# Kernel optimization log

Hardware: AMD Instinct MI355X
Metric: run time of the kernel (lower is better)

The kernel has to match this reference:

```python
import jax, jax.numpy as jnp
import numpy as np

N_NODES = 100000
N_EDGES = 1600000
IN_CH = 64
OUT_CH = 64
NUM_K = 9  # (degree+1)^dim = 3*3 quadratic B-spline taps; equals prod(kernel_size) here


def _quad_basis(v):
    # torch_spline_conv quadratic basis for k_mod in {0,1,2}; v = frac(pseudo*(K-deg)) = pseudo here
    return jnp.stack([0.5 * v * v - v + 0.5,
                      -v * v + v + 0.5,
                      0.5 * v * v], axis=-1)  # [E,3]


def spline_conv(x, src, dst, pseudo, W, root, bias, n_nodes):
    # W: [9, C_in, C_out]; basis B: [E, 9]
    b0 = _quad_basis(pseudo[:, 0])          # [E,3]
    b1 = _quad_basis(pseudo[:, 1])          # [E,3]
    B = (b0[:, :, None] * b1[:, None, :]).reshape(pseudo.shape[0], NUM_K)  # [E,9]
    x_src = x[src]                           # gather [E, C_in]
    msg = B[:, 0:1] * (x_src @ W[0])
    for k in range(1, NUM_K):                # fixed small loop over kernel taps
        msg = msg + B[:, k:k + 1] * (x_src @ W[k])
    out = jax.ops.segment_sum(msg, dst, num_segments=n_nodes)  # scatter-add at targets
    return out + x @ root + bias


def setup_inputs() -> dict:
    key = jax.random.key(0)
    ks = jax.random.split(key, 10)
    x = jax.random.normal(ks[0], (N_NODES, IN_CH), dtype=jnp.float32)
    edge_index = jax.random.randint(ks[1], (2, N_EDGES), 0, N_NODES, dtype=jnp.int64)
    pseudo = jax.random.uniform(ks[2], (N_EDGES, 2), dtype=jnp.float32)
    s1 = 1.0 / np.sqrt(IN_CH * NUM_K)
    s2 = 1.0 / np.sqrt(OUT_CH * NUM_K)
    W1 = jax.random.normal(ks[3], (NUM_K, IN_CH, OUT_CH), dtype=jnp.float32) * s1
    root1 = jax.random.normal(ks[4], (IN_CH, OUT_CH), dtype=jnp.float32) * s1
    b1 = jax.random.normal(ks[5], (OUT_CH,), dtype=jnp.float32) * 0.01
    W2 = jax.random.normal(ks[6], (NUM_K, OUT_CH, OUT_CH), dtype=jnp.float32) * s2
    root2 = jax.random.normal(ks[7], (OUT_CH, OUT_CH), dtype=jnp.float32) * s2
    b2 = jax.random.normal(ks[8], (OUT_CH,), dtype=jnp.float32) * 0.01
    return {"x": x, "edge_index": edge_index, "pseudo": pseudo,
            "W1": W1, "root1": root1, "b1": b1,
            "W2": W2, "root2": root2, "b2": b2}


def reference(x, edge_index, pseudo, W1, root1, b1, W2, root2, b2):
    src, dst = edge_index[0], edge_index[1]  # PyG: aggregate messages at target
    h = jax.nn.relu(spline_conv(x, src, dst, pseudo, W1, root1, b1, N_NODES))
    h = jax.nn.relu(spline_conv(h, src, dst, pseudo, W2, root2, b2, N_NODES))
    return h
```

## Files before the change

### kernel.cpp

```cpp
#include <hip/hip_runtime.h>
#include <stdint.h>

typedef __attribute__((ext_vector_type(8))) short bf16x8;
typedef __attribute__((ext_vector_type(4))) float f32x4;

__device__ __forceinline__ float bf2f(unsigned short u) {
  union { unsigned int i; float f; } x; x.i = ((unsigned int)u) << 16; return x.f;
}
__device__ __forceinline__ unsigned short f2bf(float f) {
  union { float f; unsigned int i; } x; x.f = f;
  unsigned int i = x.i;
  return (unsigned short)((i + 0x7FFFu + ((i >> 16) & 1u)) >> 16);
}
__device__ __forceinline__ float f16lo(unsigned int u) {
  union { unsigned short s; _Float16 h; } x; x.s = (unsigned short)(u & 0xFFFFu);
  return (float)x.h;
}
__device__ __forceinline__ float f16hi(unsigned int u) {
  union { unsigned short s; _Float16 h; } x; x.s = (unsigned short)(u >> 16);
  return (float)x.h;
}
__device__ __forceinline__ unsigned int packf16(float a, float b) {
  union { unsigned short s; _Float16 h; } x, y;
  x.h = (_Float16)a; y.h = (_Float16)b;
  return (unsigned int)x.s | ((unsigned int)y.s << 16);
}


__global__ void count_kernel(const int* __restrict__ ei, int E, int* __restrict__ counts) {
  int e = blockIdx.x * blockDim.x + threadIdx.x;
  if (e < E) atomicAdd(&counts[ei[E + e]], 1);
}

__global__ void scan1_kernel(const int* __restrict__ counts, int n, int* __restrict__ bsum) {
  int i = blockIdx.x * 256 + threadIdx.x;
  int v = (i < n) ? counts[i] : 0;
  int lane = threadIdx.x & 63, w = threadIdx.x >> 6;
  for (int d = 32; d > 0; d >>= 1) v += __shfl_down(v, d, 64);
  __shared__ int ws[4];
  if (lane == 0) ws[w] = v;
  __syncthreads();
  if (threadIdx.x == 0) bsum[blockIdx.x] = ws[0] + ws[1] + ws[2] + ws[3];
}

__global__ void scan2_kernel(int* __restrict__ bsum, int G) {
  int t = threadIdx.x;
  int c = (G + 511) >> 9;
  int lo = min(t * c, G), hi = min(lo + c, G);
  int s = 0;
  for (int i = lo; i < hi; ++i) s += bsum[i];
  int lane = t & 63, w = t >> 6;
  int incl = s;
  for (int d = 1; d < 64; d <<= 1) { int u = __shfl_up(incl, d, 64); if (lane >= d) incl += u; }
  __shared__ int wsum[8];
  if (lane == 63) wsum[w] = incl;
  __syncthreads();
  int wpre = 0;
  for (int i = 0; i < w; ++i) wpre += wsum[i];
  int excl = wpre + incl - s;
  for (int i = lo; i < hi; ++i) { int v = bsum[i]; bsum[i] = excl; excl += v; }
}

__global__ void scan3_kernel(const int* __restrict__ counts, int n, const int* __restrict__ bsum,
                             int* __restrict__ offsets, int* __restrict__ cursor, int total) {
  int i = blockIdx.x * 256 + threadIdx.x;
  int v = (i < n) ? counts[i] : 0;
  int lane = threadIdx.x & 63, w = threadIdx.x >> 6;
  int incl = v;
  for (int d = 1; d < 64; d <<= 1) { int u = __shfl_up(incl, d, 64); if (lane >= d) incl += u; }
  __shared__ int wsum[4];
  if (lane == 63) wsum[w] = incl;
  __syncthreads();
  int pre = bsum[blockIdx.x];
  for (int j = 0; j < w; ++j) pre += wsum[j];
  if (i < n) {
    int excl = pre + incl - v;
    offsets[i] = excl;
    cursor[i] = excl;
  }
  if (i == 0) offsets[n] = total;
}


__global__ void fill_kernel(const int* __restrict__ ei, const float* __restrict__ pseudo,
                            int E, int* __restrict__ cursor, uint4* __restrict__ recs) {
  int e = blockIdx.x * blockDim.x + threadIdx.x;
  if (e >= E) return;
  int d = ei[E + e];
  int s = ei[e];
  float2 uv = ((const float2*)pseudo)[e];
  float u = uv.x, v = uv.y;
  float b0 = 0.5f * u * u - u + 0.5f, b1 = -u * u + u + 0.5f, b2 = 0.5f * u * u;
  float c0 = 0.5f * v * v - v + 0.5f, c1 = -v * v + v + 0.5f, c2 = 0.5f * v * v;
  int p = atomicAdd(&cursor[d], 1);
  uint4 r;
  r.x = ((unsigned int)s) << 7;
  r.y = packf16(b0, b1);
  r.z = packf16(b2, c0);
  r.w = packf16(c1, c2);
  recs[p] = r;
}


__global__ void wconv_kernel(const float* __restrict__ W, const float* __restrict__ root,
                             unsigned short* __restrict__ Wt) {
  int i = blockIdx.x * blockDim.x + threadIdx.x;
  if (i >= 640 * 64) return;
  int co = i / 640, r = i % 640;
  float v = (r < 576) ? W[r * 64 + co] : root[(r - 576) * 64 + co];
  Wt[i] = f2bf(v);
}


__global__ void xconv_kernel(const float4* __restrict__ x4, ushort4* __restrict__ xh4, int n4) {
  int i = blockIdx.x * blockDim.x + threadIdx.x;
  if (i < n4) {
    float4 v = x4[i];
    ushort4 o;
    o.x = f2bf(v.x); o.y = f2bf(v.y); o.z = f2bf(v.z); o.w = f2bf(v.w);
    xh4[i] = o;
  }
}


#define SROW 648
#define CAP 288

#define UNPACK_FMA(RY, RZ, RW, XV)                                 \
  {                                                                \
    float b0 = f16lo(RY), b1 = f16hi(RY), b2 = f16lo(RZ);          \
    float c0 = f16hi(RZ), c1 = f16lo(RW), c2 = f16hi(RW);          \
    float t0 = b0 * (XV), t1 = b1 * (XV), t2 = b2 * (XV);          \
    a0 += t0 * c0; a1 += t0 * c1; a2 += t0 * c2;                   \
    a3 += t1 * c0; a4 += t1 * c1; a5 += t1 * c2;                   \
    a6 += t2 * c0; a7 += t2 * c1; a8 += t2 * c2;                   \
  }

template <bool OUTBF16>
__global__ __launch_bounds__(512) void fused_kernel(const int* __restrict__ offsets,
                                                    const uint4* __restrict__ recs,
                                                    const unsigned short* __restrict__ Xh,
                                                    const unsigned short* __restrict__ Wt,
                                                    const float* __restrict__ bias,
                                                    void* __restrict__ outv, int N) {
  __shared__ __align__(16) short sA[16 * SROW];
  __shared__ __align__(16) uint4 sRec[CAP];
  __shared__ __align__(16) unsigned short sXg[CAP * 64];
  int tid = threadIdx.x, w = tid >> 6, lane = tid & 63;
  int nodeBase = blockIdx.x * 16;
  int nTop = min(nodeBase + 16, N);
  const char* Xb = (const char*)Xh;
  unsigned int laneB = (unsigned int)lane * 2u;

  int blockBeg = offsets[nodeBase];
  int blockEnd = offsets[nTop];
  int stage = min(blockEnd - blockBeg, CAP);

  for (int i = tid; i < stage; i += 512) sRec[i] = recs[(size_t)blockBeg + i];
  __syncthreads();
  {
    int chunk = tid & 7;
    int rbase = tid >> 3;
    for (int r0 = 0; r0 < stage; r0 += 64) {
      int r = r0 + rbase;
      if (r < stage) {
        unsigned int so = sRec[r].x;
        uint4 v = *(const uint4*)(Xb + so + chunk * 16);
        *(uint4*)((char*)sXg + r * 128 + chunk * 16) = v;
      }
    }
  }
  __syncthreads();

#pragma unroll
  for (int t = 0; t < 2; ++t) {
    int row = w * 2 + t;
    int n = nodeBase + row;
    if (n < N) {
      int beg = __builtin_amdgcn_readfirstlane(offsets[n]);
      int end = __builtin_amdgcn_readfirstlane(offsets[n + 1]);
      unsigned short selfu = Xh[(size_t)n * 64 + lane];
      float a0 = 0.f, a1 = 0.f, a2 = 0.f, a3 = 0.f, a4 = 0.f,
            a5 = 0.f, a6 = 0.f, a7 = 0.f, a8 = 0.f;
      int lbeg = beg - blockBeg;
      int lend = end - blockBeg;
      int lcap = min(lend, CAP);
      int m = lcap - lbeg;
      for (int j0 = 0; j0 < m; j0 += 4) {
#pragma unroll
        for (int k = 0; k < 4; ++k) {
          int idx = j0 + k;
          int le = lbeg + (idx < m ? idx : 0);
          uint4 r = sRec[le];
          float xv = bf2f(sXg[le * 64 + lane]);
          if (idx >= m) { r.y = 0u; r.z = 0u; r.w = 0u; }
          UNPACK_FMA(r.y, r.z, r.w, xv)
        }
      }
      for (int j = (lbeg > lcap ? lbeg : lcap); j < lend; ++j) {
        uint4 r = recs[(size_t)blockBeg + j];
        float xv = bf2f(*(const unsigned short*)(Xb + r.x + laneB));
        UNPACK_FMA(r.y, r.z, r.w, xv)
      }
      int rb = row * SROW;
      sA[rb + 0 * 64 + lane] = (short)f2bf(a0);
      sA[rb + 1 * 64 + lane] = (short)f2bf(a1);
      sA[rb + 2 * 64 + lane] = (short)f2bf(a2);
      sA[rb + 3 * 64 + lane] = (short)f2bf(a3);
      sA[rb + 4 * 64 + lane] = (short)f2bf(a4);
      sA[rb + 5 * 64 + lane] = (short)f2bf(a5);
      sA[rb + 6 * 64 + lane] = (short)f2bf(a6);
      sA[rb + 7 * 64 + lane] = (short)f2bf(a7);
      sA[rb + 8 * 64 + lane] = (short)f2bf(a8);
      sA[rb + 576 + lane] = (short)selfu;
    }
  }
  __syncthreads();

  if (w < 4) {
    int r15 = lane & 15, kg = lane >> 4;
    f32x4 acc = {0.f, 0.f, 0.f, 0.f};
#pragma unroll
    for (int kk = 0; kk < 20; ++kk) {
      int kbase = kk * 32 + kg * 8;
      bf16x8 af = *(const bf16x8*)(&sA[r15 * SROW + kbase]);
      bf16x8 bfr = *(const bf16x8*)(Wt + (size_t)(w * 16 + r15) * 640 + kbase);
      acc = __builtin_amdgcn_mfma_f32_16x16x32_bf16(af, bfr, acc, 0, 0, 0);
    }
    int col = w * 16 + r15;
    float bv = bias[col];
    int row0 = kg * 4;
#pragma unroll
    for (int r = 0; r < 4; ++r) {
      int node = nodeBase + row0 + r;
      if (node < N) {
        float val = fmaxf(acc[r] + bv, 0.f);
        size_t idx = (size_t)node * 64 + col;
        if (OUTBF16) ((unsigned short*)outv)[idx] = f2bf(val);
        else ((float*)outv)[idx] = val;
      }
    }
  }
}


extern "C" void kernel_launch(void* const* d_in, const int* in_sizes, int n_in,
                              void* d_out, int out_size, void* d_ws, size_t ws_size,
                              hipStream_t stream) {
  const float* x = (const float*)d_in[0];
  const int* ei = (const int*)d_in[1];
  const float* pseudo = (const float*)d_in[2];
  const float* W1 = (const float*)d_in[3];
  const float* root1 = (const float*)d_in[4];
  const float* b1 = (const float*)d_in[5];
  const float* W2 = (const float*)d_in[6];
  const float* root2 = (const float*)d_in[7];
  const float* b2 = (const float*)d_in[8];

  const int N = in_sizes[0] / 64;
  const int E = in_sizes[1] / 2;
  const int G = (N + 255) / 256;

  char* p = (char*)d_ws;
  auto carve = [&](size_t bytes) -> void* {
    void* r = (void*)p;
    p += (bytes + 255) & ~(size_t)255;
    return r;
  };
  int* counts = (int*)carve((size_t)N * 4);
  int* offsets = (int*)carve((size_t)(N + 1) * 4);
  int* cursor = (int*)carve((size_t)N * 4);
  int* bsum = (int*)carve((size_t)G * 4);
  uint4* recs = (uint4*)carve((size_t)E * 16);
  unsigned short* Wt1 = (unsigned short*)carve(640 * 64 * 2);
  unsigned short* Wt2 = (unsigned short*)carve(640 * 64 * 2);
  unsigned short* h = (unsigned short*)carve((size_t)N * 64 * 2);
  unsigned short* xh = (unsigned short*)carve((size_t)N * 64 * 2);
  (void)ws_size;

  hipMemsetAsync(counts, 0, (size_t)N * 4, stream);
  count_kernel<<<(E + 255) / 256, 256, 0, stream>>>(ei, E, counts);
  scan1_kernel<<<G, 256, 0, stream>>>(counts, N, bsum);
  scan2_kernel<<<1, 512, 0, stream>>>(bsum, G);
  scan3_kernel<<<G, 256, 0, stream>>>(counts, N, bsum, offsets, cursor, E);
  fill_kernel<<<(E + 255) / 256, 256, 0, stream>>>(ei, pseudo, E, cursor, recs);
  wconv_kernel<<<160, 256, 0, stream>>>(W1, root1, Wt1);
  wconv_kernel<<<160, 256, 0, stream>>>(W2, root2, Wt2);
  xconv_kernel<<<(N * 16 + 255) / 256, 256, 0, stream>>>((const float4*)x, (ushort4*)xh, N * 16);

  int FB = (N + 15) / 16;
  fused_kernel<true><<<FB, 512, 0, stream>>>(offsets, recs, xh, Wt1, b1, (void*)h, N);
  fused_kernel<false><<<FB, 512, 0, stream>>>(offsets, recs, h, Wt2, b2, d_out, N);
}
```

Baseline: 520.8 us.

## Split block edges evenly across waves with LDS atomic flush per destination

Each block's edges are now divided evenly among the 8 waves instead of one wave per destination row. This targets load imbalance from skewed in-degrees. Each wave accumulates the 9 basis-weighted sums and flushes them to an fp32 LDS tile with atomic adds whenever the destination changes, using destination low bits packed into the record. The staged gathered-X buffer is removed in favour of direct global gathers with software double-buffering, CAP is raised, and the LDS tile is converted to bf16 before the MFMA. The trade is extra LDS atomics, more global-gather latency, and fp32 LDS storage.

```diff
diff --git a/kernel.cpp b/kernel.cpp
--- a/kernel.cpp
+++ b/kernel.cpp
@@ -24,6 +24,11 @@
   union { unsigned short s; _Float16 h; } x, y;
   x.h = (_Float16)a; y.h = (_Float16)b;
   return (unsigned int)x.s | ((unsigned int)y.s << 16);
+}
+__device__ __forceinline__ unsigned int cvtpk_bf16(float lo, float hi) {
+  unsigned int d;
+  asm("v_cvt_pk_bf16_f32 %0, %1, %2" : "=v"(d) : "v"(lo), "v"(hi));
+  return d;
 }
 
 
@@ -94,7 +99,7 @@
   float c0 = 0.5f * v * v - v + 0.5f, c1 = -v * v + v + 0.5f, c2 = 0.5f * v * v;
   int p = atomicAdd(&cursor[d], 1);
   uint4 r;
-  r.x = ((unsigned int)s) << 7;
+  r.x = (((unsigned int)s) << 7) | ((unsigned int)d & 127u);
   r.y = packf16(b0, b1);
   r.z = packf16(b2, c0);
   r.w = packf16(c1, c2);
@@ -123,8 +128,8 @@
 }
 
 
-#define SROW 648
-#define CAP 288
+#define SAFROW 644
+#define CAP 384
 
 #define UNPACK_FMA(RY, RZ, RW, XV)                                 \
   {                                                                \
@@ -136,16 +141,58 @@
     a6 += t2 * c0; a7 += t2 * c1; a8 += t2 * c2;                   \
   }
 
+#define FLUSH(C)                                                             \
+  {                                                                          \
+    float* fb_ = &sAf[(C) * SAFROW + lane];                                  \
+    atomicAdd(fb_ + 0,   a0); atomicAdd(fb_ + 64,  a1);                      \
+    atomicAdd(fb_ + 128, a2); atomicAdd(fb_ + 192, a3);                      \
+    atomicAdd(fb_ + 256, a4); atomicAdd(fb_ + 320, a5);                      \
+    atomicAdd(fb_ + 384, a6); atomicAdd(fb_ + 448, a7);                      \
+    atomicAdd(fb_ + 512, a8);                                                \
+    a0 = a1 = a2 = a3 = a4 = a5 = a6 = a7 = a8 = 0.f;                        \
+  }
+
+#define LOADG(J, R0, R1, R2, R3, X0, X1, X2, X3)                             \
+  {                                                                          \
+    R0 = sRec[(J)]; R1 = sRec[(J) + 1]; R2 = sRec[(J) + 2]; R3 = sRec[(J) + 3]; \
+    X0 = *(const unsigned short*)(Xb + (R0.x & 0xFFFFFF80u) + laneB);        \
+    X1 = *(const unsigned short*)(Xb + (R1.x & 0xFFFFFF80u) + laneB);        \
+    X2 = *(const unsigned short*)(Xb + (R2.x & 0xFFFFFF80u) + laneB);        \
+    X3 = *(const unsigned short*)(Xb + (R3.x & 0xFFFFFF80u) + laneB);        \
+  }
+
+#define PROCG(R0, R1, R2, R3, X0, X1, X2, X3)                                \
+  {                                                                          \
+    int d0_ = __builtin_amdgcn_readfirstlane(R0.x) & 15;                     \
+    int d1_ = __builtin_amdgcn_readfirstlane(R1.x) & 15;                     \
+    int d2_ = __builtin_amdgcn_readfirstlane(R2.x) & 15;                     \
+    int d3_ = __builtin_amdgcn_readfirstlane(R3.x) & 15;                     \
+    if (d0_ == cur && d1_ == cur && d2_ == cur && d3_ == cur) {              \
+      UNPACK_FMA(R0.y, R0.z, R0.w, bf2f(X0))                                 \
+      UNPACK_FMA(R1.y, R1.z, R1.w, bf2f(X1))                                 \
+      UNPACK_FMA(R2.y, R2.z, R2.w, bf2f(X2))                                 \
+      UNPACK_FMA(R3.y, R3.z, R3.w, bf2f(X3))                                 \
+    } else {                                                                 \
+      if (d0_ != cur) { FLUSH(cur) cur = d0_; }                              \
+      UNPACK_FMA(R0.y, R0.z, R0.w, bf2f(X0))                                 \
+      if (d1_ != cur) { FLUSH(cur) cur = d1_; }                              \
+      UNPACK_FMA(R1.y, R1.z, R1.w, bf2f(X1))                                 \
+      if (d2_ != cur) { FLUSH(cur) cur = d2_; }                              \
+      UNPACK_FMA(R2.y, R2.z, R2.w, bf2f(X2))                                 \
+      if (d3_ != cur) { FLUSH(cur) cur = d3_; }                              \
+      UNPACK_FMA(R3.y, R3.z, R3.w, bf2f(X3))                                 \
+    }                                                                        \
+  }
+
 template <bool OUTBF16>
-__global__ __launch_bounds__(512) void fused_kernel(const int* __restrict__ offsets,
-                                                    const uint4* __restrict__ recs,
-                                                    const unsigned short* __restrict__ Xh,
-                                                    const unsigned short* __restrict__ Wt,
-                                                    const float* __restrict__ bias,
-                                                    void* __restrict__ outv, int N) {
-  __shared__ __align__(16) short sA[16 * SROW];
+__global__ __launch_bounds__(512, 6) void fused_kernel(const int* __restrict__ offsets,
+                                                       const uint4* __restrict__ recs,
+                                                       const unsigned short* __restrict__ Xh,
+                                                       const unsigned short* __restrict__ Wt,
+                                                       const float* __restrict__ bias,
+                                                       void* __restrict__ outv, int N) {
+  __shared__ __align__(16) float sAf[16 * SAFROW];
   __shared__ __align__(16) uint4 sRec[CAP];
-  __shared__ __align__(16) unsigned short sXg[CAP * 64];
   int tid = threadIdx.x, w = tid >> 6, lane = tid & 63;
   int nodeBase = blockIdx.x * 16;
   int nTop = min(nodeBase + 16, N);
@@ -157,62 +204,72 @@
   int stage = min(blockEnd - blockBeg, CAP);
 
   for (int i = tid; i < stage; i += 512) sRec[i] = recs[(size_t)blockBeg + i];
-  __syncthreads();
-  {
-    int chunk = tid & 7;
-    int rbase = tid >> 3;
-    for (int r0 = 0; r0 < stage; r0 += 64) {
-      int r = r0 + rbase;
-      if (r < stage) {
-        unsigned int so = sRec[r].x;
-        uint4 v = *(const uint4*)(Xb + so + chunk * 16);
-        *(uint4*)((char*)sXg + r * 128 + chunk * 16) = v;
-      }
-    }
-  }
-  __syncthreads();
-
+  for (int i = tid; i < 16 * 144; i += 512) {
+    int r = i / 144, c = i - r * 144;
+    *(f32x4*)(&sAf[r * SAFROW + c * 4]) = (f32x4){0.f, 0.f, 0.f, 0.f};
+  }
 #pragma unroll
   for (int t = 0; t < 2; ++t) {
     int row = w * 2 + t;
     int n = nodeBase + row;
-    if (n < N) {
-      int beg = __builtin_amdgcn_readfirstlane(offsets[n]);
-      int end = __builtin_amdgcn_readfirstlane(offsets[n + 1]);
-      unsigned short selfu = Xh[(size_t)n * 64 + lane];
+    if (n < nTop) sAf[row * SAFROW + 576 + lane] = bf2f(Xh[(size_t)n * 64 + lane]);
+  }
+  __syncthreads();
+
+  {
+    int chunk = (stage + 7) >> 3;
+    int cBeg = w * chunk;
+    int cEnd = min(stage, cBeg + chunk);
+    if (cBeg < cEnd) {
       float a0 = 0.f, a1 = 0.f, a2 = 0.f, a3 = 0.f, a4 = 0.f,
             a5 = 0.f, a6 = 0.f, a7 = 0.f, a8 = 0.f;
-      int lbeg = beg - blockBeg;
-      int lend = end - blockBeg;
-      int lcap = min(lend, CAP);
-      int m = lcap - lbeg;
-      for (int j0 = 0; j0 < m; j0 += 4) {
+      int cur = __builtin_amdgcn_readfirstlane(sRec[cBeg].x) & 15;
+      int i = cBeg;
+      int nfull = (cEnd - cBeg) >> 2;
+      uint4 r0, r1, r2, r3, s0, s1, s2, s3;
+      unsigned short px0, px1, px2, px3, py0, py1, py2, py3;
+      if (nfull > 0) { LOADG(i, r0, r1, r2, r3, px0, px1, px2, px3) }
+      int g = 0;
+      while (g < nfull) {
+        if (g + 1 < nfull) { LOADG(i + 4, s0, s1, s2, s3, py0, py1, py2, py3) }
+        PROCG(r0, r1, r2, r3, px0, px1, px2, px3)
+        i += 4; ++g;
+        if (g >= nfull) break;
+        if (g + 1 < nfull) { LOADG(i + 4, r0, r1, r2, r3, px0, px1, px2, px3) }
+        PROCG(s0, s1, s2, s3, py0, py1, py2, py3)
+        i += 4; ++g;
+      }
+      for (; i < cEnd; ++i) {
+        uint4 rr = sRec[i];
+        unsigned short xv = *(const unsigned short*)(Xb + (rr.x & 0xFFFFFF80u) + laneB);
+        int dd = __builtin_amdgcn_readfirstlane(rr.x) & 15;
+        if (dd != cur) { FLUSH(cur) cur = dd; }
+        UNPACK_FMA(rr.y, rr.z, rr.w, bf2f(xv))
+      }
+      FLUSH(cur)
+    }
+    if (blockEnd - blockBeg > CAP) {
+      int gcap = blockBeg + CAP;
 #pragma unroll
-        for (int k = 0; k < 4; ++k) {
-          int idx = j0 + k;
-          int le = lbeg + (idx < m ? idx : 0);
-          uint4 r = sRec[le];
-          float xv = bf2f(sXg[le * 64 + lane]);
-          if (idx >= m) { r.y = 0u; r.z = 0u; r.w = 0u; }
-          UNPACK_FMA(r.y, r.z, r.w, xv)
+      for (int t = 0; t < 2; ++t) {
+        int row = w * 2 + t;
+        int n = nodeBase + row;
+        if (n < nTop) {
+          int beg = __builtin_amdgcn_readfirstlane(offsets[n]);
+          int end = __builtin_amdgcn_readfirstlane(offsets[n + 1]);
+          int s = beg > gcap ? beg : gcap;
+          if (s < end) {
+            float a0 = 0.f, a1 = 0.f, a2 = 0.f, a3 = 0.f, a4 = 0.f,
+                  a5 = 0.f, a6 = 0.f, a7 = 0.f, a8 = 0.f;
+            for (int j = s; j < end; ++j) {
+              uint4 rr = recs[j];
+              unsigned short xv = *(const unsigned short*)(Xb + (rr.x & 0xFFFFFF80u) + laneB);
+              UNPACK_FMA(rr.y, rr.z, rr.w, bf2f(xv))
+            }
+            FLUSH(row)
+          }
         }
       }
-      for (int j = (lbeg > lcap ? lbeg : lcap); j < lend; ++j) {
-        uint4 r = recs[(size_t)blockBeg + j];
-        float xv = bf2f(*(const unsigned short*)(Xb + r.x + laneB));
-        UNPACK_FMA(r.y, r.z, r.w, xv)
-      }
-      int rb = row * SROW;
-      sA[rb + 0 * 64 + lane] = (short)f2bf(a0);
-      sA[rb + 1 * 64 + lane] = (short)f2bf(a1);
-      sA[rb + 2 * 64 + lane] = (short)f2bf(a2);
-      sA[rb + 3 * 64 + lane] = (short)f2bf(a3);
-      sA[rb + 4 * 64 + lane] = (short)f2bf(a4);
-      sA[rb + 5 * 64 + lane] = (short)f2bf(a5);
-      sA[rb + 6 * 64 + lane] = (short)f2bf(a6);
-      sA[rb + 7 * 64 + lane] = (short)f2bf(a7);
-      sA[rb + 8 * 64 + lane] = (short)f2bf(a8);
-      sA[rb + 576 + lane] = (short)selfu;
     }
   }
   __syncthreads();
@@ -223,9 +280,15 @@
 #pragma unroll
     for (int kk = 0; kk < 20; ++kk) {
       int kbase = kk * 32 + kg * 8;
-      bf16x8 af = *(const bf16x8*)(&sA[r15 * SROW + kbase]);
+      f32x4 v0 = *(const f32x4*)(&sAf[r15 * SAFROW + kbase]);
+      f32x4 v1 = *(const f32x4*)(&sAf[r15 * SAFROW + kbase + 4]);
+      union { unsigned int u[4]; bf16x8 v8; } af;
+      af.u[0] = cvtpk_bf16(v0[0], v0[1]);
+      af.u[1] = cvtpk_bf16(v0[2], v0[3]);
+      af.u[2] = cvtpk_bf16(v1[0], v1[1]);
+      af.u[3] = cvtpk_bf16(v1[2], v1[3]);
       bf16x8 bfr = *(const bf16x8*)(Wt + (size_t)(w * 16 + r15) * 640 + kbase);
-      acc = __builtin_amdgcn_mfma_f32_16x16x32_bf16(af, bfr, acc, 0, 0, 0);
+      acc = __builtin_amdgcn_mfma_f32_16x16x32_bf16(af.v8, bfr, acc, 0, 0, 0);
     }
     int col = w * 16 + r15;
     float bv = bias[col];
```

Measured after the change: 1.188 ms. 128% more time.

## Stream edges per warp across four nodes with software-pipelined gathers

Applied to the files above, without the earlier changes.

Drops the LDS staging of edge records and gathered source rows. Each wave now walks the contiguous edge range of four consecutive nodes, with records and feature loads prefetched three edges ahead in a rotating pipeline. A packed low-bit destination tag in the record marks node boundaries, and the accumulators are flushed to shared memory whenever the node changes. Blocks shrink to 256 threads and LDS use drops, which allows more blocks per CU, but the scalar tag check and a zero-init pass add work in the inner loop.

```diff
diff --git a/kernel.cpp b/kernel.cpp
--- a/kernel.cpp
+++ b/kernel.cpp
@@ -94,7 +94,7 @@
   float c0 = 0.5f * v * v - v + 0.5f, c1 = -v * v + v + 0.5f, c2 = 0.5f * v * v;
   int p = atomicAdd(&cursor[d], 1);
   uint4 r;
-  r.x = ((unsigned int)s) << 7;
+  r.x = (((unsigned int)s) << 7) | ((unsigned int)d & 127u);
   r.y = packf16(b0, b1);
   r.z = packf16(b2, c0);
   r.w = packf16(c1, c2);
@@ -124,100 +124,111 @@
 
 
 #define SROW 648
-#define CAP 288
-
-#define UNPACK_FMA(RY, RZ, RW, XV)                                 \
+
+#define GX(R) (*(const unsigned short*)(Xb + ((R).x & 0xFFFFFF80u) + laneB))
+
+#define FLUSHROW(C)                                                \
   {                                                                \
-    float b0 = f16lo(RY), b1 = f16hi(RY), b2 = f16lo(RZ);          \
-    float c0 = f16hi(RZ), c1 = f16lo(RW), c2 = f16hi(RW);          \
-    float t0 = b0 * (XV), t1 = b1 * (XV), t2 = b2 * (XV);          \
+    int rb_ = (C) * SROW + lane;                                   \
+    sA[rb_ + 0 * 64] = (short)f2bf(a0);                            \
+    sA[rb_ + 1 * 64] = (short)f2bf(a1);                            \
+    sA[rb_ + 2 * 64] = (short)f2bf(a2);                            \
+    sA[rb_ + 3 * 64] = (short)f2bf(a3);                            \
+    sA[rb_ + 4 * 64] = (short)f2bf(a4);                            \
+    sA[rb_ + 5 * 64] = (short)f2bf(a5);                            \
+    sA[rb_ + 6 * 64] = (short)f2bf(a6);                            \
+    sA[rb_ + 7 * 64] = (short)f2bf(a7);                            \
+    sA[rb_ + 8 * 64] = (short)f2bf(a8);                            \
+    a0 = a1 = a2 = a3 = a4 = a5 = a6 = a7 = a8 = 0.f;              \
+  }
+
+#define PROC(R, XU)                                                \
+  {                                                                \
+    int d_ = __builtin_amdgcn_readfirstlane((R).x) & 15;           \
+    if (d_ != cur) { FLUSHROW(cur) cur = d_; }                     \
+    float xv = bf2f((unsigned short)(XU));                         \
+    float b0 = f16lo((R).y), b1 = f16hi((R).y), b2 = f16lo((R).z); \
+    float c0 = f16hi((R).z), c1 = f16lo((R).w), c2 = f16hi((R).w); \
+    float t0 = b0 * xv, t1 = b1 * xv, t2 = b2 * xv;                \
     a0 += t0 * c0; a1 += t0 * c1; a2 += t0 * c2;                   \
     a3 += t1 * c0; a4 += t1 * c1; a5 += t1 * c2;                   \
     a6 += t2 * c0; a7 += t2 * c1; a8 += t2 * c2;                   \
   }
 
 template <bool OUTBF16>
-__global__ __launch_bounds__(512) void fused_kernel(const int* __restrict__ offsets,
+__global__ __launch_bounds__(256) void fused_kernel(const int* __restrict__ offsets,
                                                     const uint4* __restrict__ recs,
                                                     const unsigned short* __restrict__ Xh,
                                                     const unsigned short* __restrict__ Wt,
                                                     const float* __restrict__ bias,
                                                     void* __restrict__ outv, int N) {
   __shared__ __align__(16) short sA[16 * SROW];
-  __shared__ __align__(16) uint4 sRec[CAP];
-  __shared__ __align__(16) unsigned short sXg[CAP * 64];
   int tid = threadIdx.x, w = tid >> 6, lane = tid & 63;
   int nodeBase = blockIdx.x * 16;
-  int nTop = min(nodeBase + 16, N);
   const char* Xb = (const char*)Xh;
   unsigned int laneB = (unsigned int)lane * 2u;
 
-  int blockBeg = offsets[nodeBase];
-  int blockEnd = offsets[nTop];
-  int stage = min(blockEnd - blockBeg, CAP);
-
-  for (int i = tid; i < stage; i += 512) sRec[i] = recs[(size_t)blockBeg + i];
-  __syncthreads();
   {
-    int chunk = tid & 7;
-    int rbase = tid >> 3;
-    for (int r0 = 0; r0 < stage; r0 += 64) {
-      int r = r0 + rbase;
-      if (r < stage) {
-        unsigned int so = sRec[r].x;
-        uint4 v = *(const uint4*)(Xb + so + chunk * 16);
-        *(uint4*)((char*)sXg + r * 128 + chunk * 16) = v;
+    f32x4 z = {0.f, 0.f, 0.f, 0.f};
+    for (int i = tid; i < 16 * 36; i += 256) {
+      int r = i / 36, c = i - r * 36;
+      *(f32x4*)((char*)sA + r * (SROW * 2) + c * 16) = z;
+    }
+  }
+#pragma unroll
+  for (int t = 0; t < 4; ++t) {
+    int row = w * 4 + t;
+    int n = nodeBase + row;
+    if (n < N) sA[row * SROW + 576 + lane] = (short)Xh[(size_t)n * 64 + lane];
+  }
+
+  {
+    int n0 = nodeBase + w * 4;
+    int n1 = min(n0 + 4, N);
+    if (n0 < N) {
+      int j = __builtin_amdgcn_readfirstlane(offsets[n0]);
+      int jEnd = __builtin_amdgcn_readfirstlane(offsets[n1]);
+      if (j < jEnd) {
+        int last = jEnd - 1;
+        float a0 = 0.f, a1 = 0.f, a2 = 0.f, a3 = 0.f, a4 = 0.f,
+              a5 = 0.f, a6 = 0.f, a7 = 0.f, a8 = 0.f;
+        uint4 rA = recs[j];
+        uint4 rB = recs[min(j + 1, last)];
+        uint4 rC = recs[min(j + 2, last)];
+        unsigned int xA = GX(rA);
+        unsigned int xB = GX(rB);
+        unsigned int xC;
+        int cur = __builtin_amdgcn_readfirstlane(rA.x) & 15;
+        for (;;) {
+          {
+            uint4 rN = recs[min(j + 3, last)];
+            xC = GX(rC);
+            PROC(rA, xA)
+            rA = rN;
+            if (++j >= jEnd) break;
+          }
+          {
+            uint4 rN = recs[min(j + 3, last)];
+            xA = GX(rA);
+            PROC(rB, xB)
+            rB = rN;
+            if (++j >= jEnd) break;
+          }
+          {
+            uint4 rN = recs[min(j + 3, last)];
+            xB = GX(rB);
+            PROC(rC, xC)
+            rC = rN;
+            if (++j >= jEnd) break;
+          }
+        }
+        FLUSHROW(cur)
       }
     }
   }
   __syncthreads();
 
-#pragma unroll
-  for (int t = 0; t < 2; ++t) {
-    int row = w * 2 + t;
-    int n = nodeBase + row;
-    if (n < N) {
-      int beg = __builtin_amdgcn_readfirstlane(offsets[n]);
-      int end = __builtin_amdgcn_readfirstlane(offsets[n + 1]);
-      unsigned short selfu = Xh[(size_t)n * 64 + lane];
-      float a0 = 0.f, a1 = 0.f, a2 = 0.f, a3 = 0.f, a4 = 0.f,
-            a5 = 0.f, a6 = 0.f, a7 = 0.f, a8 = 0.f;
-      int lbeg = beg - blockBeg;
-      int lend = end - blockBeg;
-      int lcap = min(lend, CAP);
-      int m = lcap - lbeg;
-      for (int j0 = 0; j0 < m; j0 += 4) {
-#pragma unroll
-        for (int k = 0; k < 4; ++k) {
-          int idx = j0 + k;
-          int le = lbeg + (idx < m ? idx : 0);
-          uint4 r = sRec[le];
-          float xv = bf2f(sXg[le * 64 + lane]);
-          if (idx >= m) { r.y = 0u; r.z = 0u; r.w = 0u; }
-          UNPACK_FMA(r.y, r.z, r.w, xv)
-        }
-      }
-      for (int j = (lbeg > lcap ? lbeg : lcap); j < lend; ++j) {
-        uint4 r = recs[(size_t)blockBeg + j];
-        float xv = bf2f(*(const unsigned short*)(Xb + r.x + laneB));
-        UNPACK_FMA(r.y, r.z, r.w, xv)
-      }
-      int rb = row * SROW;
-      sA[rb + 0 * 64 + lane] = (short)f2bf(a0);
-      sA[rb + 1 * 64 + lane] = (short)f2bf(a1);
-      sA[rb + 2 * 64 + lane] = (short)f2bf(a2);
-      sA[rb + 3 * 64 + lane] = (short)f2bf(a3);
-      sA[rb + 4 * 64 + lane] = (short)f2bf(a4);
-      sA[rb + 5 * 64 + lane] = (short)f2bf(a5);
-      sA[rb + 6 * 64 + lane] = (short)f2bf(a6);
-      sA[rb + 7 * 64 + lane] = (short)f2bf(a7);
-      sA[rb + 8 * 64 + lane] = (short)f2bf(a8);
-      sA[rb + 576 + lane] = (short)selfu;
-    }
-  }
-  __syncthreads();
-
-  if (w < 4) {
+  {
     int r15 = lane & 15, kg = lane >> 4;
     f32x4 acc = {0.f, 0.f, 0.f, 0.f};
 #pragma unroll
@@ -289,6 +300,6 @@
   xconv_kernel<<<(N * 16 + 255) / 256, 256, 0, stream>>>((const float4*)x, (ushort4*)xh, N * 16);
 
   int FB = (N + 15) / 16;
-  fused_kernel<true><<<FB, 512, 0, stream>>>(offsets, recs, xh, Wt1, b1, (void*)h, N);
-  fused_kernel<false><<<FB, 512, 0, stream>>>(offsets, recs, h, Wt2, b2, d_out, N);
-}
+  fused_kernel<true><<<FB, 256, 0, stream>>>(offsets, recs, xh, Wt1, b1, (void*)h, N);
+  fused_kernel<false><<<FB, 256, 0, stream>>>(offsets, recs, h, Wt2, b2, d_out, N);
+}
```

New measurement: 460.6 us. 11.6% less time.
